# Kernel optimization log

Hardware: AMD Instinct MI355X
Metric: run time of the kernel (lower is better)

Reference implementation:

```python
import jax, jax.numpy as jnp
import numpy as np

NUM_Q = 100000; NUM_C = 1000; D = 128; BS = 128; SEQ = 128
QN = 4; CN = 10; NQC = 4; AGG_HOPS = 2; RANK_K = 10
NEG = jnp.float32(-1e9)


def setup_inputs() -> dict:
    key = jax.random.key(0)
    ks = iter(jax.random.split(key, 40))
    def nrm(shape, scale=0.05):
        return jax.random.normal(next(ks), shape, dtype=jnp.float32) * scale
    inp = {}
    inp['question_seq'] = jax.random.randint(next(ks), (BS, SEQ), 0, NUM_Q, dtype=jnp.int32)
    inp['correct_seq'] = jax.random.randint(next(ks), (BS, SEQ), 0, 2, dtype=jnp.int32)
    inp['mask_seq'] = jnp.ones((BS, SEQ), dtype=jnp.int32)
    inp['question_neighbors'] = jax.random.randint(next(ks), (NUM_Q, QN), 0, NUM_C, dtype=jnp.int32)
    inp['concept_neighbors'] = jax.random.randint(next(ks), (NUM_C, CN), 0, NUM_Q, dtype=jnp.int32)
    inp['qc_table'] = jax.random.randint(next(ks), (NUM_Q, NQC), 0, NUM_C, dtype=jnp.int32)
    inp['Eq'] = nrm((NUM_Q, D), 1.0)
    inp['Ec'] = nrm((NUM_C, D), 1.0)
    inp['Er'] = nrm((2, D), 1.0)
    inp['W_ih1'] = nrm((3 * D, 2 * D)); inp['W_hh1'] = nrm((3 * D, D))
    inp['b_ih1'] = nrm((3 * D,)); inp['b_hh1'] = nrm((3 * D,))
    inp['W_ih2'] = nrm((3 * D, D)); inp['W_hh2'] = nrm((3 * D, D))
    inp['b_ih2'] = nrm((3 * D,)); inp['b_hh2'] = nrm((3 * D,))
    inp['W_agg'] = nrm((AGG_HOPS, D, D)); inp['b_agg'] = nrm((AGG_HOPS, D))
    inp['W_agg_last'] = nrm((D, D)); inp['b_agg_last'] = nrm((D,))
    inp['Wq'] = nrm((D, D)); inp['bq'] = nrm((D,))
    inp['Wk'] = nrm((D, D)); inp['bk'] = nrm((D,))
    inp['Ww'] = nrm((1, 2 * D)); inp['bw'] = nrm((1,))
    inp['h1_init'] = nrm((BS, D)); inp['h2_init'] = nrm((BS, D))
    return inp


def _gru(x, h, W_ih, W_hh, b_ih, b_hh):
    gi = x @ W_ih.T + b_ih
    gh = h @ W_hh.T + b_hh
    ir, iz, i_n = jnp.split(gi, 3, axis=-1)
    hr, hz, hn = jnp.split(gh, 3, axis=-1)
    r = jax.nn.sigmoid(ir + hr)
    z = jax.nn.sigmoid(iz + hz)
    n = jnp.tanh(i_n + r * hn)
    return (1 - z) * n + z * h


def _forward(question_seq, correct_seq, mask_seq, question_neighbors, concept_neighbors, qc_table,
             Eq, Ec, Er, W_ih1, W_hh1, b_ih1, b_hh1, W_ih2, W_hh2, b_ih2, b_hh2,
             W_agg, b_agg, W_agg_last, b_agg_last, Wq, bq, Wk, bk, Ww, bw, h1_init, h2_init):
    bs, seq_len = question_seq.shape
    d = Eq.shape[1]
    # detached question embeddings of the whole history (recap scoring key)
    K_all = jax.lax.stop_gradient(Eq[question_seq])  # [bs, seq, d]
    Wh, Wqc = Ww[:, :d], Ww[:, d:]  # MLP_W split over [state; question_concept]

    def predict(qc, hist, hist_mask):
        # qc: [bs,nqc,d], hist: [bs,ns,d], hist_mask: [bs,ns]
        Kp = qc @ Wk.T + bk                     # MLP_key
        Qp = hist @ Wq.T + bq                   # MLP_query
        logits = jnp.einsum('bsd,bqd->bsq', Qp, Kp)
        logits = jnp.where(hist_mask[:, :, None], logits, NEG)
        w = jax.nn.softmax(logits.reshape(bs, -1), axis=1)
        # pairwise sigmoid(MLP_W([h; e])) without materializing the concat
        v = jax.nn.sigmoid((hist @ Wh[0])[:, :, None] + (qc @ Wqc[0])[:, None, :] + bw[0])
        return jnp.sum(w * v.reshape(bs, -1), axis=1)

    def step(carry, t):
        h1, h2, state_hist, y_hat = carry
        q_t = jnp.take(question_seq, t, axis=1)
        r_t = jnp.take(correct_seq, t, axis=1)
        m_t = jnp.take(mask_seq, t, axis=1) != 0
        # --- 2-hop GNN aggregation (question -> concept -> question) ---
        n1 = question_neighbors[q_t]            # [bs, QN] concept ids
        n2 = concept_neighbors[n1]              # [bs, QN, CN] question ids
        emb = [Eq[q_t], Ec[n1], Eq[n2]]
        for i in range(AGG_HOPS):
            for j in range(AGG_HOPS - i):
                s = jnp.mean(emb[j + 1], axis=-2) + emb[j]
                emb[j] = jnp.tanh(s @ W_agg[j].T + b_agg[j])
        agg = jnp.tanh(emb[0] @ W_agg_last.T + b_agg_last)
        emb_q = jnp.where(m_t[:, None], agg, Eq[q_t])
        # --- GRU state updates (dropout in eval mode = identity) ---
        h1n = _gru(jnp.concatenate([emb_q, Er[r_t]], axis=1), h1, W_ih1, W_hh1, b_ih1, b_hh1)
        g2 = _gru(h1n, h2, W_ih2, W_hh2, b_ih2, b_hh2)
        # --- next question + its concepts ---
        q_next = jnp.take(question_seq, t + 1, axis=1)
        qc = jnp.concatenate([Eq[q_next][:, None], Ec[qc_table[q_next]]], axis=1)  # [bs, 1+NQC, d]
        # --- soft recap: top-k history states by detached embedding similarity ---
        scores = jnp.einsum('bsd,bd->bs', K_all, jax.lax.stop_gradient(Eq[q_next]))
        valid = jnp.arange(seq_len) < t
        scores = jnp.where(valid[None, :], scores, NEG)
        top_vals, top_idx = jax.lax.top_k(scores, RANK_K)
        sel = jnp.take_along_axis(state_hist, top_idx[:, :, None], axis=1)  # [bs, k, d]
        sel_mask = top_vals > NEG / 2
        hist = jnp.concatenate([g2[:, None], sel], axis=1)
        hist_mask = jnp.concatenate([jnp.ones((bs, 1), dtype=bool), sel_mask], axis=1)
        p = predict(qc, hist, hist_mask)
        idx = jnp.where(t == 0, 0, t + 1)  # original writes y_hat[:,0] at t==0
        y_hat = y_hat.at[:, idx].set(p)
        # h2 / state_history NOT updated at t==0 (original `continue`)
        upd = t > 0
        h2n = jnp.where(upd, g2, h2)
        state_hist = jnp.where(upd, state_hist.at[:, t].set(g2), state_hist)
        return (h1n, h2n, state_hist, y_hat), None

    init = (h1_init, h2_init,
            jnp.zeros((bs, seq_len, d), jnp.float32),
            jnp.zeros((bs, seq_len), jnp.float32))
    (_, _, _, y_hat), _ = jax.lax.scan(jax.checkpoint(step), init, jnp.arange(seq_len - 1))
    return y_hat


def reference(question_seq, correct_seq, mask_seq, question_neighbors, concept_neighbors, qc_table,
              Eq, Ec, Er, W_ih1, W_hh1, b_ih1, b_hh1, W_ih2, W_hh2, b_ih2, b_hh2,
              W_agg, b_agg, W_agg_last, b_agg_last, Wq, bq, Wk, bk, Ww, bw, h1_init, h2_init):
    return _forward(question_seq, correct_seq, mask_seq, question_neighbors, concept_neighbors, qc_table,
                    Eq, Ec, Er, W_ih1, W_hh1, b_ih1, b_hh1, W_ih2, W_hh2, b_ih2, b_hh2,
                    W_agg, b_agg, W_agg_last, b_agg_last, Wq, bq, Wk, bk, Ww, bw, h1_init, h2_init)
```

## Files before the change

kernel.cpp:

```cpp
#include <hip/hip_runtime.h>

#define DD 128
#define BSZ 128
#define SEQL 128
#define TST 127
#define QNN 4
#define CNN 10
#define NQCC 4
#define RKK 10
#define NEGV -1000000000.0f

#define OFF_WTA0    0
#define OFF_WTA1    16384
#define OFF_WTAL    32768
#define OFF_WTIH1A  49152
#define OFF_ERIH1   98304
#define OFF_MT      99072
#define OFF_WPACK   115456
#define OFF_ECA0    189184
#define OFF_E1C     317184
#define OFF_KQC     445184
#define OFF_VQCC    509184
#define OFF_KBC     510184
#define OFF_U       511184
#define OFF_W2      511312
#define OFF_C0      511440
#define OFF_GRAM    511488
#define OFF_GI1     511488
#define OFF_KQ0     6753792
#define OFF_VQC0    7802368
#define OFF_KB0     7818752
#define OFF_TIX     7835136
#define OFF_TMSK    7997696
#define OFF_CID     8160256

#define XI(e) ((e) + (((e) >> 5) << 2))
#define PH(e) ((((e) >> 5) * 40) + ((e) & 31))
#define PU(e) ((((e) >> 5) * 20) + (((e) & 31) >> 1))

typedef __fp16 h2 __attribute__((ext_vector_type(2)));

__device__ __forceinline__ float sigm(float x) { return 1.0f / (1.0f + __expf(-x)); }
__device__ __forceinline__ unsigned pkh(float a, float b) {
  h2 v; v.x = (__fp16)a; v.y = (__fp16)b;
  return __builtin_bit_cast(unsigned, v);
}
__device__ __forceinline__ float fd2(float acc, unsigned w, h2 x) {
  return __builtin_amdgcn_fdot2(__builtin_bit_cast(h2, w), x, acc, false);
}
__device__ __forceinline__ float fd2u(float acc, unsigned w, unsigned x) {
  return __builtin_amdgcn_fdot2(__builtin_bit_cast(h2, w), __builtin_bit_cast(h2, x), acc, false);
}
__device__ __forceinline__ void bar() {
  asm volatile("s_waitcnt lgkmcnt(0)" ::: "memory");
  __builtin_amdgcn_s_barrier();
  asm volatile("" ::: "memory");
}

__global__ __launch_bounds__(256) void k_prep(
    const float* __restrict__ W_hh1, const float* __restrict__ W_ih2,
    const float* __restrict__ W_hh2, const float* __restrict__ W_agg,
    const float* __restrict__ W_agg_last, const float* __restrict__ W_ih1,
    const float* __restrict__ Er, float* __restrict__ ws) {
  int idx = blockIdx.x * 256 + threadIdx.x;
  const int TOT = 172800;
  for (int o = idx; o < TOT; o += gridDim.x * 256) {
    int r = o;
    if (r < 16384) { int j = r >> 7, i = r & 127; ws[OFF_WTA0 + r] = W_agg[i * 128 + j]; continue; }
    r -= 16384;
    if (r < 16384) { int j = r >> 7, i = r & 127; ws[OFF_WTA1 + r] = W_agg[16384 + i * 128 + j]; continue; }
    r -= 16384;
    if (r < 16384) { int j = r >> 7, i = r & 127; ws[OFF_WTAL + r] = W_agg_last[i * 128 + j]; continue; }
    r -= 16384;
    if (r < 49152) { int j = r / 384, i = r % 384; ws[OFF_WTIH1A + r] = W_ih1[i * 256 + j]; continue; }
    r -= 49152;
    if (r < 768) {
      int rr = r / 384, i2 = r % 384;
      float a = 0.f;
      for (int j = 0; j < 128; ++j) a += Er[rr * 128 + j] * W_ih1[i2 * 256 + 128 + j];
      ws[OFF_ERIH1 + r] = a; continue;
    }
    r -= 768;
    {
      int n = r & 3; int q = r >> 2;
      int i = q & 127; q >>= 7;
      int kk = q & 3; q >>= 2;
      int jc = q & 3; int c = q >> 2;
      int j0 = jc * 32 + kk * 8 + n * 2;
      const float* row;
      if (c < 3) row = W_hh1 + (size_t)(c * 128 + i) * 128;
      else if (c < 6) row = W_ih2 + (size_t)((c - 3) * 128 + i) * 128;
      else row = W_hh2 + (size_t)((c - 6) * 128 + i) * 128;
      ((unsigned*)ws)[OFF_WPACK + r] = pkh(row[j0], row[j0 + 1]);
    }
  }
}

__global__ __launch_bounds__(128) void k_mqk(
    const float* __restrict__ Wq, const float* __restrict__ Wk,
    const float* __restrict__ bq, const float* __restrict__ bk,
    float* __restrict__ ws) {
  int j = blockIdx.x;
  int tid = threadIdx.x;
  if (j < 128) {
    __shared__ float wkc[128];
    wkc[tid] = Wk[tid * 128 + j];
    __syncthreads();
    float a = 0.f;
    for (int l = 0; l < 128; ++l) a = fmaf(Wq[l * 128 + tid], wkc[l], a);
    ws[OFF_MT + j * 128 + tid] = a;
  } else if (j == 128) {
    float a = 0.f;
    for (int l = 0; l < 128; ++l) a = fmaf(Wq[l * 128 + tid], bk[l], a);
    ws[OFF_U + tid] = a;
  } else {
    float a = 0.f;
    for (int l = 0; l < 128; ++l) a = fmaf(bq[l], Wk[l * 128 + tid], a);
    ws[OFF_W2 + tid] = a;
    __shared__ float sc[128];
    sc[tid] = bq[tid] * bk[tid];
    __syncthreads();
    if (tid == 0) { float s = 0.f; for (int l = 0; l < 128; ++l) s += sc[l]; ws[OFF_C0] = s; }
  }
}

__global__ __launch_bounds__(128) void k_concept(
    const int* __restrict__ cnbr, const float* __restrict__ Eq,
    const float* __restrict__ Ec, const float* __restrict__ b_agg,
    const float* __restrict__ Ww, float* __restrict__ ws) {
  int c = blockIdx.x;
  int tid = threadIdx.x;
  __shared__ int s_nb[CNN];
  __shared__ float s_v[DD], s_ec[DD], s_t2[DD], s_w2[DD], s_kb2[DD];
  if (tid < CNN) s_nb[tid] = cnbr[c * CNN + tid];
  __syncthreads();
  float ec = Ec[c * DD + tid];
  float cm = 0.f;
#pragma unroll
  for (int l = 0; l < CNN; ++l) cm += Eq[(size_t)s_nb[l] * DD + tid];
  s_ec[tid] = ec;
  s_v[tid] = cm * 0.1f + ec;
  __syncthreads();
  const float* WtA0 = ws + OFF_WTA0;
  const float* WtA1 = ws + OFF_WTA1;
  const float* MT = ws + OFF_MT;
  float a1 = 0.f, a0 = 0.f, kq = 0.f;
#pragma unroll 8
  for (int j = 0; j < DD; ++j) {
    a1 += WtA1[j * DD + tid] * s_v[j];
    a0 += WtA0[j * DD + tid] * s_ec[j];
    kq += MT[j * DD + tid] * s_ec[j];
  }
  ws[OFF_E1C + c * DD + tid] = tanhf(a1 + b_agg[DD + tid]);
  ws[OFF_ECA0 + c * DD + tid] = a0;
  s_t2[tid] = kq + ws[OFF_U + tid];
  s_w2[tid] = s_ec[tid] * Ww[128 + tid];
  s_kb2[tid] = s_ec[tid] * ws[OFF_W2 + tid];
  __syncthreads();
  if (tid < 64) {
    ((unsigned*)ws)[OFF_KQC + c * 64 + tid] = pkh(s_t2[2 * tid], s_t2[2 * tid + 1]);
    float pa = s_w2[tid] + s_w2[tid + 64];
    float pb = s_kb2[tid] + s_kb2[tid + 64];
    for (int off = 32; off > 0; off >>= 1) { pa += __shfl_down(pa, off); pb += __shfl_down(pb, off); }
    if (tid == 0) { ws[OFF_VQCC + c] = pa; ws[OFF_KBC + c] = pb + ws[OFF_C0]; }
  }
}

__global__ __launch_bounds__(256) void k_gram(
    const int* __restrict__ qseq, const float* __restrict__ Eq,
    const float* __restrict__ Ww, float* __restrict__ ws) {
  int b = blockIdx.x;
  int tid = threadIdx.x;
  __shared__ float sX[128][129];
  __shared__ float s_tmp[2][8][DD];
  __shared__ int sq[SEQL];
  __shared__ float sU[DD], sWqc[DD], sW2[DD];
  if (tid < 128) {
    sq[tid] = qseq[b * SEQL + tid];
    sU[tid] = ws[OFF_U + tid];
    sWqc[tid] = Ww[128 + tid];
    sW2[tid] = ws[OFF_W2 + tid];
  }
  __syncthreads();
  for (int o = tid; o < 128 * 32; o += 256) {
    int s = o >> 5, p = o & 31;
    float4 v = ((const float4*)(Eq + (size_t)sq[s] * DD))[p];
    sX[s][p * 4] = v.x; sX[s][p * 4 + 1] = v.y; sX[s][p * 4 + 2] = v.z; sX[s][p * 4 + 3] = v.w;
  }
  __syncthreads();
  {
    int r0 = (tid >> 4) * 8, c0 = (tid & 15) * 8;
    float acc[8][8];
#pragma unroll
    for (int u = 0; u < 8; ++u)
#pragma unroll
      for (int v = 0; v < 8; ++v) acc[u][v] = 0.f;
    for (int k = 0; k < 128; ++k) {
      float a[8], bb[8];
#pragma unroll
      for (int u = 0; u < 8; ++u) { a[u] = sX[r0 + u][k]; bb[u] = sX[c0 + u][k]; }
#pragma unroll
      for (int u = 0; u < 8; ++u)
#pragma unroll
        for (int v = 0; v < 8; ++v) acc[u][v] = fmaf(a[u], bb[v], acc[u][v]);
    }
    float* gb = ws + OFF_GRAM + (size_t)b * 16384;
#pragma unroll
    for (int u = 0; u < 8; ++u) {
      float4 v0 = {acc[u][0], acc[u][1], acc[u][2], acc[u][3]};
      float4 v1 = {acc[u][4], acc[u][5], acc[u][6], acc[u][7]};
      ((float4*)(gb + (size_t)(r0 + u) * 128 + c0))[0] = v0;
      ((float4*)(gb + (size_t)(r0 + u) * 128 + c0 + 4))[0] = v1;
    }
  }
  {
    const float* MT = ws + OFF_MT;
    unsigned* KQ0 = (unsigned*)ws + OFF_KQ0;
    int i = tid & 127, half = tid >> 7;
    int s0 = half * 64;
    for (int sb = 0; sb < 64; sb += 8) {
      float acc[8];
#pragma unroll
      for (int u = 0; u < 8; ++u) acc[u] = 0.f;
      for (int j = 0; j < DD; ++j) {
        float w = MT[j * DD + i];
#pragma unroll
        for (int u = 0; u < 8; ++u) acc[u] = fmaf(w, sX[s0 + sb + u][j], acc[u]);
      }
      __syncthreads();
#pragma unroll
      for (int u = 0; u < 8; ++u) s_tmp[half][u][i] = acc[u] + sU[i];
      __syncthreads();
      for (int o = tid; o < 16 * 64; o += 256) {
        int rr = o >> 6, e = o & 63;
        int hh = rr >> 3, uu = rr & 7;
        int s = hh * 64 + sb + uu;
        KQ0[((size_t)b * 128 + s) * 64 + e] = pkh(s_tmp[hh][uu][2 * e], s_tmp[hh][uu][2 * e + 1]);
      }
      __syncthreads();
    }
  }
  if (tid < 128) {
    float a = 0.f, kb = 0.f;
    for (int j = 0; j < DD; ++j) {
      float xv = sX[tid][j];
      a = fmaf(xv, sWqc[j], a);
      kb = fmaf(xv, sW2[j], kb);
    }
    ws[OFF_VQC0 + b * 128 + tid] = a;
    ws[OFF_KB0 + b * 128 + tid] = kb + ws[OFF_C0];
  }
}

__global__ __launch_bounds__(128) void k_topk(
    const int* __restrict__ qseq, const int* __restrict__ qctab,
    float* __restrict__ ws) {
  int* tix = (int*)(ws + OFF_TIX);
  int* tmsk = (int*)(ws + OFF_TMSK);
  int* cid = (int*)(ws + OFF_CID);
  int tid = threadIdx.x;
  int lane = tid & 63, wv = tid >> 6;
  int bt = blockIdx.x * 2 + wv;
  int b = bt / TST, t = bt - b * TST;
  if (lane < 5) {
    int qn = qseq[b * SEQL + t + 1];
    cid[(b * 128 + t + 1) * 5 + lane] = (lane == 0) ? qn : qctab[qn * NQCC + lane - 1];
  }
  const float* grow = ws + OFF_GRAM + ((size_t)b * 128 + (t + 1)) * 128;
  float v0 = (lane < t) ? grow[lane] : NEGV;
  float v1 = (lane + 64 < t) ? grow[lane + 64] : NEGV;
  for (int k = 0; k < RKK; ++k) {
    float bv = v0; int bi = lane;
    if (v1 > bv) { bv = v1; bi = lane + 64; }
    for (int off = 32; off > 0; off >>= 1) {
      float ov = __shfl_down(bv, off);
      int oi = __shfl_down(bi, off);
      if (ov > bv || (ov == bv && oi < bi)) { bv = ov; bi = oi; }
    }
    bv = __shfl(bv, 0); bi = __shfl(bi, 0);
    if (lane == 0) {
      tix[bt * RKK + k] = bi;
      tmsk[bt * RKK + k] = (bv > NEGV * 0.5f) ? 1 : 0;
    }
    if (bi == lane) v0 = -__builtin_inff();
    if (bi == lane + 64) v1 = -__builtin_inff();
  }
}

__global__ __launch_bounds__(128) void k_agg(
    const int* __restrict__ qseq, const int* __restrict__ rseq,
    const int* __restrict__ mseq, const int* __restrict__ qnbr,
    const float* __restrict__ Eq, const float* __restrict__ b_agg,
    const float* __restrict__ b_agg_last, const float* __restrict__ b_ih1,
    float* __restrict__ ws) {
  int blk = blockIdx.x;
  int b = blk >> 4, g = blk & 15;
  int t0 = g * 8;
  int nu = (t0 + 8 <= TST) ? 8 : (TST - t0);
  int tid = threadIdx.x;
  __shared__ float s_a[8][DD], s_b[8][DD], s_c[8][DD];
  __shared__ int s_q[8], s_r[8], s_m[8];
  __shared__ int s_n1[8][QNN];
  if (tid < 8) {
    int ok = tid < nu;
    int idx = b * SEQL + (ok ? (t0 + tid) : 0);
    s_q[tid] = qseq[idx];
    s_r[tid] = ok ? rseq[idx] : 0;
    s_m[tid] = ok ? mseq[idx] : 0;
  }
  __syncthreads();
  if (tid < 32) { int u = tid >> 2, k = tid & 3; s_n1[u][k] = qnbr[s_q[u] * QNN + k]; }
  for (int o = tid; o < 8 * 32; o += 128) {
    int u = o >> 5, p = o & 31;
    float4 v = ((const float4*)(Eq + (size_t)s_q[u] * DD))[p];
    s_a[u][p * 4] = v.x; s_a[u][p * 4 + 1] = v.y; s_a[u][p * 4 + 2] = v.z; s_a[u][p * 4 + 3] = v.w;
  }
  __syncthreads();
  const float* WtA0 = ws + OFF_WTA0;
  const float* WtAL = ws + OFF_WTAL;
  const float* WtIH1A = ws + OFF_WTIH1A;
  const float* EcA0 = ws + OFF_ECA0;
  const float* E1C = ws + OFF_E1C;
  float acc[8];
#pragma unroll
  for (int u = 0; u < 8; ++u) acc[u] = 0.f;
  for (int j = 0; j < DD; ++j) {
    float w = WtA0[j * DD + tid];
#pragma unroll
    for (int u = 0; u < 8; ++u) acc[u] = fmaf(w, s_a[u][j], acc[u]);
  }
  float bat = b_agg[tid];
#pragma unroll
  for (int u = 0; u < 8; ++u) {
    int n0 = s_n1[u][0], n1 = s_n1[u][1], n2 = s_n1[u][2], n3 = s_n1[u][3];
    float pre0 = 0.25f * (EcA0[n0 * DD + tid] + EcA0[n1 * DD + tid] + EcA0[n2 * DD + tid] + EcA0[n3 * DD + tid]);
    float e0 = tanhf(acc[u] + pre0 + bat);
    float e1m = 0.25f * (E1C[n0 * DD + tid] + E1C[n1 * DD + tid] + E1C[n2 * DD + tid] + E1C[n3 * DD + tid]);
    s_b[u][tid] = e1m + e0;
  }
  __syncthreads();
#pragma unroll
  for (int u = 0; u < 8; ++u) acc[u] = 0.f;
  for (int j = 0; j < DD; ++j) {
    float w = WtA0[j * DD + tid];
#pragma unroll
    for (int u = 0; u < 8; ++u) acc[u] = fmaf(w, s_b[u][j], acc[u]);
  }
#pragma unroll
  for (int u = 0; u < 8; ++u) s_c[u][tid] = tanhf(acc[u] + bat);
  __syncthreads();
#pragma unroll
  for (int u = 0; u < 8; ++u) acc[u] = 0.f;
  for (int j = 0; j < DD; ++j) {
    float w = WtAL[j * DD + tid];
#pragma unroll
    for (int u = 0; u < 8; ++u) acc[u] = fmaf(w, s_c[u][j], acc[u]);
  }
  float balt = b_agg_last[tid];
#pragma unroll
  for (int u = 0; u < 8; ++u) {
    float aggv = tanhf(acc[u] + balt);
    s_b[u][tid] = s_m[u] ? aggv : s_a[u][tid];
  }
  __syncthreads();
  float g0[8], g1[8], g2[8];
#pragma unroll
  for (int u = 0; u < 8; ++u) { g0[u] = 0.f; g1[u] = 0.f; g2[u] = 0.f; }
  for (int j = 0; j < DD; ++j) {
    float w0 = WtIH1A[j * 384 + tid];
    float w1 = WtIH1A[j * 384 + 128 + tid];
    float w2 = WtIH1A[j * 384 + 256 + tid];
#pragma unroll
    for (int u = 0; u < 8; ++u) {
      float x = s_b[u][j];
      g0[u] = fmaf(w0, x, g0[u]);
      g1[u] = fmaf(w1, x, g1[u]);
      g2[u] = fmaf(w2, x, g2[u]);
    }
  }
  for (int u = 0; u < nu; ++u) {
    const float* ErI = ws + OFF_ERIH1 + s_r[u] * 384;
    float* gi1 = ws + OFF_GI1 + (size_t)(b * TST + t0 + u) * 384;
    gi1[tid] = g0[u] + ErI[tid] + b_ih1[tid];
    gi1[128 + tid] = g1[u] + ErI[128 + tid] + b_ih1[128 + tid];
    gi1[256 + tid] = g2[u] + ErI[256 + tid] + b_ih1[256 + tid];
  }
}

__global__ __launch_bounds__(512, 2) void k_seq(
    const float* __restrict__ b_hh1, const float* __restrict__ b_ih2,
    const float* __restrict__ b_hh2, const float* __restrict__ Ww,
    const float* __restrict__ bw, const float* __restrict__ h1i,
    const float* __restrict__ h2i, float* __restrict__ ws,
    float* __restrict__ out) {
  const int tid = threadIdx.x;
  const int b = blockIdx.x;
  const int i = tid >> 2, jc = tid & 3;
  const int lane = tid & 63, wv = tid >> 6;
  const int bt0 = b * TST;

  const float4* gi1f4 = (const float4*)(ws + OFF_GI1);
  const unsigned* KQ0 = (const unsigned*)ws + OFF_KQ0;
  const unsigned* KQC = (const unsigned*)ws + OFF_KQC;
  const float* vqc0_all = ws + OFF_VQC0;
  const float* vqcC_all = ws + OFF_VQCC;
  const float* kb0_all = ws + OFF_KB0;
  const float* kbC_all = ws + OFF_KBC;
  const int* tix_all = (const int*)(ws + OFF_TIX);
  const int* tmsk_all = (const int*)(ws + OFF_TMSK);
  const int* cid_all = (const int*)(ws + OFF_CID);
  const uint4* wp = (const uint4*)((const unsigned*)ws + OFF_WPACK);

  __shared__ float s_h1f[2][144], s_g2f[2][144], s_h2f[144];
  __shared__ unsigned s_h1pk[2][80], s_g2pk[2][80], s_h2pk[80];
  __shared__ unsigned qph_pk[SEQL * 66];
  __shared__ unsigned s_Kq[2][5 * 66];
  __shared__ float s_gi1[384];
  __shared__ float s_vhh[SEQL];
  __shared__ float s_logit[64];
  __shared__ float s_bhh1[384], s_bih2[384], s_bhh2[384];
  __shared__ float s_vh[11], s_vqc[2][5], s_kb[2][5], s_bw;
  __shared__ int s_tix[RKK], s_hm[11], s_cidn[5];

  uint4 wgt[9][4];
#pragma unroll
  for (int c = 0; c < 9; ++c)
#pragma unroll
    for (int kk = 0; kk < 4; ++kk)
      wgt[c][kk] = wp[((c * 4 + jc) * 4 + kk) * 128 + i];
#pragma unroll
  for (int c = 0; c < 9; ++c)
#pragma unroll
    for (int kk = 0; kk < 4; ++kk)
      asm volatile("" : "+v"(wgt[c][kk].x), "+v"(wgt[c][kk].y),
                        "+v"(wgt[c][kk].z), "+v"(wgt[c][kk].w));

  if (tid < 384) { s_bhh1[tid] = b_hh1[tid]; s_bih2[tid] = b_ih2[tid]; s_bhh2[tid] = b_hh2[tid]; }
  if (tid < 128) {
    float h1v = h1i[b * DD + tid], h2v = h2i[b * DD + tid];
    s_h1f[0][XI(tid)] = h1v;
    ((__fp16*)s_h1pk[0])[PH(tid)] = (__fp16)h1v;
    s_h2f[XI(tid)] = h2v;
    ((__fp16*)s_h2pk)[PH(tid)] = (__fp16)h2v;
    s_vhh[tid] = 0.f;
  }
  if (tid >= 55 && tid < 64) s_logit[tid] = NEGV;
  float wh_lo = 0.f, wh_hi = 0.f;
  if (wv == 7) { wh_lo = Ww[lane]; wh_hi = Ww[64 + lane]; }
  if (tid == 0) { s_bw = bw[0]; out[b * SEQL + 1] = 0.f; s_hm[0] = 1; }
  if (tid >= 296 && tid < 301) s_cidn[tid - 296] = cid_all[(b * 128 + 1) * 5 + tid - 296];
  __syncthreads();
  for (int o = tid; o < SEQL * 66; o += 512) qph_pk[o] = 0u;
  if (tid < 96) ((float4*)s_gi1)[tid] = gi1f4[(size_t)bt0 * 96 + tid];
  __syncthreads();

  for (int t = 0; t <= TST; ++t) {
    const int par = t & 1, parn = par ^ 1;
    float4 pf4 = {0.f, 0.f, 0.f, 0.f};
    unsigned pfu = 0, pfu2 = 0; int pfs = 0; float pfv = 0.f, pfkb = 0.f;

    if (t < TST) {
      const int tg = (t + 1 < TST) ? t + 1 : TST - 1;
      if (tid < 96) pf4 = gi1f4[(size_t)(bt0 + tg) * 96 + tid];
      else if (tid < 256) {
        int kx = tid - 96;
        { int s = kx >> 6, e = kx & 63;
          pfu = (s == 0) ? KQ0[(size_t)(b * 128 + t + 1) * 64 + e] : KQC[s_cidn[s] * 64 + e]; }
        { int kx2 = kx + 160; int s = kx2 >> 6, e = kx2 & 63;
          pfu2 = KQC[s_cidn[s] * 64 + e]; }
      } else if (tid < 291) {
        int k = tid - 256;
        if (k < 5) pfv = (k == 0) ? vqc0_all[b * 128 + t + 1] : vqcC_all[s_cidn[k]];
        else if (k < 10) { int s = k - 5; pfkb = (s == 0) ? kb0_all[b * 128 + t + 1] : kbC_all[s_cidn[s]]; }
        else if (k < 20) pfs = tix_all[(bt0 + t) * RKK + k - 10];
        else if (k < 30) pfs = tmsk_all[(bt0 + t) * RKK + k - 20];
        else { int tn = (t + 1 < TST) ? t + 1 : TST - 1; pfs = cid_all[(b * 128 + tn + 1) * 5 + k - 30]; }
      }
      const uint4* xp = (const uint4*)s_h1pk[par] + jc * 5;
      float a0 = 0.f, a1 = 0.f, a2 = 0.f;
#pragma unroll
      for (int kk = 0; kk < 4; ++kk) {
        uint4 xk = xp[kk];
        uint4 w;
        w = wgt[0][kk]; a0 = fd2u(a0, w.x, xk.x); a0 = fd2u(a0, w.y, xk.y); a0 = fd2u(a0, w.z, xk.z); a0 = fd2u(a0, w.w, xk.w);
        w = wgt[1][kk]; a1 = fd2u(a1, w.x, xk.x); a1 = fd2u(a1, w.y, xk.y); a1 = fd2u(a1, w.z, xk.z); a1 = fd2u(a1, w.w, xk.w);
        w = wgt[2][kk]; a2 = fd2u(a2, w.x, xk.x); a2 = fd2u(a2, w.y, xk.y); a2 = fd2u(a2, w.z, xk.z); a2 = fd2u(a2, w.w, xk.w);
      }
      a0 += __shfl_down(a0, 2); a0 += __shfl_down(a0, 1);
      a1 += __shfl_down(a1, 2); a1 += __shfl_down(a1, 1);
      a2 += __shfl_down(a2, 2); a2 += __shfl_down(a2, 1);
      if (jc == 0) {
        float r = sigm(s_gi1[i] + a0 + s_bhh1[i]);
        float z = sigm(s_gi1[128 + i] + a1 + s_bhh1[128 + i]);
        float n = tanhf(s_gi1[256 + i] + r * (a2 + s_bhh1[256 + i]));
        float h1n = (1.f - z) * n + z * s_h1f[par][XI(i)];
        s_h1f[parn][XI(i)] = h1n;
        ((__fp16*)s_h1pk[parn])[PH(i)] = (__fp16)h1n;
      }
    }
    if (t >= 1) {
      if (tid < 440) {
        int p = tid >> 3, sub = tid & 7;
        int q = p / 5, s = p - q * 5;
        const unsigned* kpr = &s_Kq[parn][s * 66 + sub * 8];
        float a = 0.f;
        if (q == 0) {
          const unsigned* g2u = s_g2pk[parn];
          int e0 = sub * 16;
#pragma unroll
          for (int k = 0; k < 8; ++k) a = fd2u(a, kpr[k], g2u[PU(e0 + 2 * k)]);
        } else {
          const unsigned* ro = qph_pk + s_tix[q - 1] * 66;
#pragma unroll
          for (int k = 0; k < 8; ++k) a = fd2u(a, ro[sub * 8 + k], kpr[k]);
        }
        a += __shfl_down(a, 4);
        a += __shfl_down(a, 2);
        a += __shfl_down(a, 1);
        if (sub == 0) s_logit[p] = s_hm[q] ? (a + s_kb[parn][s]) : NEGV;
      } else if (wv == 7) {
        float pa = s_g2f[parn][XI(lane)] * wh_lo + s_g2f[parn][XI(64 + lane)] * wh_hi;
        for (int off = 32; off > 0; off >>= 1) pa += __shfl_down(pa, off);
        if (lane == 0) s_vh[0] = pa;
        if (lane >= 16 && lane < 26) s_vh[1 + lane - 16] = s_vhh[s_tix[lane - 16]];
      }
    }
    bar();

    if (t < TST) {
      const uint4* xn = (const uint4*)s_h1pk[parn] + jc * 5;
      const uint4* xh = (t <= 1) ? ((const uint4*)s_h2pk + jc * 5)
                                 : ((const uint4*)s_g2pk[parn] + jc * 5);
      float a0 = 0.f, a1 = 0.f, a2 = 0.f, c0 = 0.f, c1 = 0.f, c2 = 0.f;
#pragma unroll
      for (int kk = 0; kk < 4; ++kk) {
        uint4 xa = xn[kk], xb = xh[kk];
        uint4 w;
        w = wgt[3][kk]; a0 = fd2u(a0, w.x, xa.x); a0 = fd2u(a0, w.y, xa.y); a0 = fd2u(a0, w.z, xa.z); a0 = fd2u(a0, w.w, xa.w);
        w = wgt[4][kk]; a1 = fd2u(a1, w.x, xa.x); a1 = fd2u(a1, w.y, xa.y); a1 = fd2u(a1, w.z, xa.z); a1 = fd2u(a1, w.w, xa.w);
        w = wgt[5][kk]; a2 = fd2u(a2, w.x, xa.x); a2 = fd2u(a2, w.y, xa.y); a2 = fd2u(a2, w.z, xa.z); a2 = fd2u(a2, w.w, xa.w);
        w = wgt[6][kk]; c0 = fd2u(c0, w.x, xb.x); c0 = fd2u(c0, w.y, xb.y); c0 = fd2u(c0, w.z, xb.z); c0 = fd2u(c0, w.w, xb.w);
        w = wgt[7][kk]; c1 = fd2u(c1, w.x, xb.x); c1 = fd2u(c1, w.y, xb.y); c1 = fd2u(c1, w.z, xb.z); c1 = fd2u(c1, w.w, xb.w);
        w = wgt[8][kk]; c2 = fd2u(c2, w.x, xb.x); c2 = fd2u(c2, w.y, xb.y); c2 = fd2u(c2, w.z, xb.z); c2 = fd2u(c2, w.w, xb.w);
      }
      a0 += __shfl_down(a0, 2); a0 += __shfl_down(a0, 1);
      a1 += __shfl_down(a1, 2); a1 += __shfl_down(a1, 1);
      a2 += __shfl_down(a2, 2); a2 += __shfl_down(a2, 1);
      c0 += __shfl_down(c0, 2); c0 += __shfl_down(c0, 1);
      c1 += __shfl_down(c1, 2); c1 += __shfl_down(c1, 1);
      c2 += __shfl_down(c2, 2); c2 += __shfl_down(c2, 1);
      if (jc == 0) {
        float r = sigm(a0 + s_bih2[i] + c0 + s_bhh2[i]);
        float z = sigm(a1 + s_bih2[128 + i] + c1 + s_bhh2[128 + i]);
        float n = tanhf(a2 + s_bih2[256 + i] + r * (c2 + s_bhh2[256 + i]));
        float h2old = (t <= 1) ? s_h2f[XI(i)] : s_g2f[parn][XI(i)];
        float g2v = (1.f - z) * n + z * h2old;
        s_g2f[par][XI(i)] = g2v;
        ((__fp16*)s_g2pk[par])[PH(i)] = (__fp16)g2v;
      }
    }
    if (t >= 1 && wv == 7) {
      float l = s_logit[lane];
      float m = l;
      for (int off = 32; off > 0; off >>= 1) m = fmaxf(m, __shfl_xor(m, off));
      float e = __expf(l - m);
      float v = 0.f;
      if (lane < 55) {
        int q = lane / 5, s = lane - q * 5;
        v = sigm(s_vh[q] + s_vqc[parn][s] + s_bw);
      }
      float num = e * v, den = e;
      for (int off = 32; off > 0; off >>= 1) { num += __shfl_xor(num, off); den += __shfl_xor(den, off); }
      if (lane == 0) out[b * SEQL + ((t - 1 == 0) ? 0 : t)] = num / den;
    }
    if (t < TST) {
      if (tid < 96) ((float4*)s_gi1)[tid] = pf4;
      else if (tid < 256) {
        int kx = tid - 96;
        { int s = kx >> 6, e = kx & 63; s_Kq[par][s * 66 + e] = pfu; }
        { int kx2 = kx + 160; int s = kx2 >> 6, e = kx2 & 63; s_Kq[par][s * 66 + e] = pfu2; }
      } else if (tid < 291) {
        int k = tid - 256;
        if (k < 5) s_vqc[par][k] = pfv;
        else if (k < 10) s_kb[par][k - 5] = pfkb;
        else if (k < 20) s_tix[k - 10] = pfs;
        else if (k < 30) s_hm[1 + k - 20] = pfs;
        else s_cidn[k - 30] = pfs;
      }
    }
    if (t >= 2 && tid >= 320 && tid < 384) {
      int k2 = tid - 320;
      qph_pk[(t - 1) * 66 + k2] = s_g2pk[parn][PU(2 * k2)];
    }
    if (t >= 2 && tid == 0) s_vhh[t - 1] = s_vh[0];
    bar();
  }
}

extern "C" void kernel_launch(void* const* d_in, const int* in_sizes, int n_in,
                              void* d_out, int out_size, void* d_ws, size_t ws_size,
                              hipStream_t stream) {
  (void)in_sizes; (void)n_in; (void)out_size; (void)ws_size;
  const int* qseq = (const int*)d_in[0];
  const int* rseq = (const int*)d_in[1];
  const int* mseq = (const int*)d_in[2];
  const int* qnbr = (const int*)d_in[3];
  const int* cnbr = (const int*)d_in[4];
  const int* qctab = (const int*)d_in[5];
  const float* Eq = (const float*)d_in[6];
  const float* Ec = (const float*)d_in[7];
  const float* Er = (const float*)d_in[8];
  const float* W_ih1 = (const float*)d_in[9];
  const float* W_hh1 = (const float*)d_in[10];
  const float* b_ih1 = (const float*)d_in[11];
  const float* b_hh1 = (const float*)d_in[12];
  const float* W_ih2 = (const float*)d_in[13];
  const float* W_hh2 = (const float*)d_in[14];
  const float* b_ih2 = (const float*)d_in[15];
  const float* b_hh2 = (const float*)d_in[16];
  const float* W_agg = (const float*)d_in[17];
  const float* b_agg = (const float*)d_in[18];
  const float* W_agg_last = (const float*)d_in[19];
  const float* b_agg_last = (const float*)d_in[20];
  const float* Wq = (const float*)d_in[21];
  const float* bq = (const float*)d_in[22];
  const float* Wk = (const float*)d_in[23];
  const float* bk = (const float*)d_in[24];
  const float* Ww = (const float*)d_in[25];
  const float* bw = (const float*)d_in[26];
  const float* h1i = (const float*)d_in[27];
  const float* h2i = (const float*)d_in[28];
  float* ws = (float*)d_ws;
  float* out = (float*)d_out;

  hipLaunchKernelGGL(k_prep, dim3(675), dim3(256), 0, stream,
                     W_hh1, W_ih2, W_hh2, W_agg, W_agg_last, W_ih1, Er, ws);
  hipLaunchKernelGGL(k_mqk, dim3(130), dim3(128), 0, stream,
                     Wq, Wk, bq, bk, ws);
  hipLaunchKernelGGL(k_concept, dim3(1000), dim3(128), 0, stream,
                     cnbr, Eq, Ec, b_agg, Ww, ws);
  hipLaunchKernelGGL(k_gram, dim3(BSZ), dim3(256), 0, stream,
                     qseq, Eq, Ww, ws);
  hipLaunchKernelGGL(k_topk, dim3(BSZ * TST / 2), dim3(128), 0, stream,
                     qseq, qctab, ws);
  hipLaunchKernelGGL(k_agg, dim3(BSZ * 16), dim3(128), 0, stream,
                     qseq, rseq, mseq, qnbr, Eq, b_agg, b_agg_last, b_ih1, ws);
  hipLaunchKernelGGL(k_seq, dim3(BSZ), dim3(512), 0, stream,
                     b_hh1, b_ih2, b_hh2, Ww, bw, h1i, h2i, ws, out);
}
```

Baseline: 617.6 us.

## Merge prep kernels, split gram kernel roles, use fast tanh

```diff
diff --git a/kernel.cpp b/kernel.cpp
--- a/kernel.cpp
+++ b/kernel.cpp
@@ -41,6 +41,12 @@
 typedef __fp16 h2 __attribute__((ext_vector_type(2)));
 
 __device__ __forceinline__ float sigm(float x) { return 1.0f / (1.0f + __expf(-x)); }
+__device__ __forceinline__ float ftanh(float x) {
+  float ax = fabsf(x);
+  float T = __expf(-2.f * ax);
+  float r = (1.f - T) * __builtin_amdgcn_rcpf(1.f + T);
+  return copysignf(r, x);
+}
 __device__ __forceinline__ unsigned pkh(float a, float b) {
   h2 v; v.x = (__fp16)a; v.y = (__fp16)b;
   return __builtin_bit_cast(unsigned, v);
@@ -61,66 +67,71 @@
     const float* __restrict__ W_hh1, const float* __restrict__ W_ih2,
     const float* __restrict__ W_hh2, const float* __restrict__ W_agg,
     const float* __restrict__ W_agg_last, const float* __restrict__ W_ih1,
-    const float* __restrict__ Er, float* __restrict__ ws) {
-  int idx = blockIdx.x * 256 + threadIdx.x;
-  const int TOT = 172800;
-  for (int o = idx; o < TOT; o += gridDim.x * 256) {
-    int r = o;
-    if (r < 16384) { int j = r >> 7, i = r & 127; ws[OFF_WTA0 + r] = W_agg[i * 128 + j]; continue; }
-    r -= 16384;
-    if (r < 16384) { int j = r >> 7, i = r & 127; ws[OFF_WTA1 + r] = W_agg[16384 + i * 128 + j]; continue; }
-    r -= 16384;
-    if (r < 16384) { int j = r >> 7, i = r & 127; ws[OFF_WTAL + r] = W_agg_last[i * 128 + j]; continue; }
-    r -= 16384;
-    if (r < 49152) { int j = r / 384, i = r % 384; ws[OFF_WTIH1A + r] = W_ih1[i * 256 + j]; continue; }
-    r -= 49152;
-    if (r < 768) {
-      int rr = r / 384, i2 = r % 384;
-      float a = 0.f;
-      for (int j = 0; j < 128; ++j) a += Er[rr * 128 + j] * W_ih1[i2 * 256 + 128 + j];
-      ws[OFF_ERIH1 + r] = a; continue;
-    }
-    r -= 768;
-    {
-      int n = r & 3; int q = r >> 2;
-      int i = q & 127; q >>= 7;
-      int kk = q & 3; q >>= 2;
-      int jc = q & 3; int c = q >> 2;
-      int j0 = jc * 32 + kk * 8 + n * 2;
-      const float* row;
-      if (c < 3) row = W_hh1 + (size_t)(c * 128 + i) * 128;
-      else if (c < 6) row = W_ih2 + (size_t)((c - 3) * 128 + i) * 128;
-      else row = W_hh2 + (size_t)((c - 6) * 128 + i) * 128;
-      ((unsigned*)ws)[OFF_WPACK + r] = pkh(row[j0], row[j0 + 1]);
-    }
-  }
-}
-
-__global__ __launch_bounds__(128) void k_mqk(
-    const float* __restrict__ Wq, const float* __restrict__ Wk,
-    const float* __restrict__ bq, const float* __restrict__ bk,
-    float* __restrict__ ws) {
-  int j = blockIdx.x;
+    const float* __restrict__ Er, const float* __restrict__ Wq,
+    const float* __restrict__ Wk, const float* __restrict__ bq,
+    const float* __restrict__ bk, float* __restrict__ ws) {
   int tid = threadIdx.x;
-  if (j < 128) {
+  if (blockIdx.x < 675) {
+    int idx = blockIdx.x * 256 + tid;
+    const int TOT = 172800;
+    for (int o = idx; o < TOT; o += 675 * 256) {
+      int r = o;
+      if (r < 16384) { int j = r >> 7, i = r & 127; ws[OFF_WTA0 + r] = W_agg[i * 128 + j]; continue; }
+      r -= 16384;
+      if (r < 16384) { int j = r >> 7, i = r & 127; ws[OFF_WTA1 + r] = W_agg[16384 + i * 128 + j]; continue; }
+      r -= 16384;
+      if (r < 16384) { int j = r >> 7, i = r & 127; ws[OFF_WTAL + r] = W_agg_last[i * 128 + j]; continue; }
+      r -= 16384;
+      if (r < 49152) { int j = r / 384, i = r % 384; ws[OFF_WTIH1A + r] = W_ih1[i * 256 + j]; continue; }
+      r -= 49152;
+      if (r < 768) {
+        int rr = r / 384, i2 = r % 384;
+        float a = 0.f;
+        for (int j = 0; j < 128; ++j) a += Er[rr * 128 + j] * W_ih1[i2 * 256 + 128 + j];
+        ws[OFF_ERIH1 + r] = a; continue;
+      }
+      r -= 768;
+      {
+        int n = r & 3; int q = r >> 2;
+        int i = q & 127; q >>= 7;
+        int kk = q & 3; q >>= 2;
+        int jc = q & 3; int c = q >> 2;
+        int j0 = jc * 32 + kk * 8 + n * 2;
+        const float* row;
+        if (c < 3) row = W_hh1 + (size_t)(c * 128 + i) * 128;
+        else if (c < 6) row = W_ih2 + (size_t)((c - 3) * 128 + i) * 128;
+        else row = W_hh2 + (size_t)((c - 6) * 128 + i) * 128;
+        ((unsigned*)ws)[OFF_WPACK + r] = pkh(row[j0], row[j0 + 1]);
+      }
+    }
+  } else {
+    int j = blockIdx.x - 675;
     __shared__ float wkc[128];
-    wkc[tid] = Wk[tid * 128 + j];
-    __syncthreads();
-    float a = 0.f;
-    for (int l = 0; l < 128; ++l) a = fmaf(Wq[l * 128 + tid], wkc[l], a);
-    ws[OFF_MT + j * 128 + tid] = a;
-  } else if (j == 128) {
-    float a = 0.f;
-    for (int l = 0; l < 128; ++l) a = fmaf(Wq[l * 128 + tid], bk[l], a);
-    ws[OFF_U + tid] = a;
-  } else {
-    float a = 0.f;
-    for (int l = 0; l < 128; ++l) a = fmaf(bq[l], Wk[l * 128 + tid], a);
-    ws[OFF_W2 + tid] = a;
     __shared__ float sc[128];
-    sc[tid] = bq[tid] * bk[tid];
-    __syncthreads();
-    if (tid == 0) { float s = 0.f; for (int l = 0; l < 128; ++l) s += sc[l]; ws[OFF_C0] = s; }
+    if (j < 128) {
+      if (tid < 128) wkc[tid] = Wk[tid * 128 + j];
+      __syncthreads();
+      if (tid < 128) {
+        float a = 0.f;
+        for (int l = 0; l < 128; ++l) a = fmaf(Wq[l * 128 + tid], wkc[l], a);
+        ws[OFF_MT + j * 128 + tid] = a;
+      }
+    } else if (j == 128) {
+      if (tid < 128) {
+        float a = 0.f;
+        for (int l = 0; l < 128; ++l) a = fmaf(Wq[l * 128 + tid], bk[l], a);
+        ws[OFF_U + tid] = a;
+      }
+    } else {
+      if (tid < 128) {
+        float a = 0.f;
+        for (int l = 0; l < 128; ++l) a = fmaf(bq[l], Wk[l * 128 + tid], a);
+        ws[OFF_W2 + tid] = a;
+        sc[tid] = bq[tid] * bk[tid];
+      }
+      __syncthreads();
+      if (tid == 0) { float s = 0.f; for (int l = 0; l < 128; ++l) s += sc[l]; ws[OFF_C0] = s; }
+    }
   }
 }
 
@@ -151,7 +162,7 @@
     a0 += WtA0[j * DD + tid] * s_ec[j];
     kq += MT[j * DD + tid] * s_ec[j];
   }
-  ws[OFF_E1C + c * DD + tid] = tanhf(a1 + b_agg[DD + tid]);
+  ws[OFF_E1C + c * DD + tid] = ftanh(a1 + b_agg[DD + tid]);
   ws[OFF_ECA0 + c * DD + tid] = a0;
   s_t2[tid] = kq + ws[OFF_U + tid];
   s_w2[tid] = s_ec[tid] * Ww[128 + tid];
@@ -169,18 +180,12 @@
 __global__ __launch_bounds__(256) void k_gram(
     const int* __restrict__ qseq, const float* __restrict__ Eq,
     const float* __restrict__ Ww, float* __restrict__ ws) {
-  int b = blockIdx.x;
+  int role = blockIdx.x >> 7;
+  int b = blockIdx.x & 127;
   int tid = threadIdx.x;
   __shared__ float sX[128][129];
-  __shared__ float s_tmp[2][8][DD];
   __shared__ int sq[SEQL];
-  __shared__ float sU[DD], sWqc[DD], sW2[DD];
-  if (tid < 128) {
-    sq[tid] = qseq[b * SEQL + tid];
-    sU[tid] = ws[OFF_U + tid];
-    sWqc[tid] = Ww[128 + tid];
-    sW2[tid] = ws[OFF_W2 + tid];
-  }
+  if (tid < 128) sq[tid] = qseq[b * SEQL + tid];
   __syncthreads();
   for (int o = tid; o < 128 * 32; o += 256) {
     int s = o >> 5, p = o & 31;
@@ -188,7 +193,7 @@
     sX[s][p * 4] = v.x; sX[s][p * 4 + 1] = v.y; sX[s][p * 4 + 2] = v.z; sX[s][p * 4 + 3] = v.w;
   }
   __syncthreads();
-  {
+  if (role == 0) {
     int r0 = (tid >> 4) * 8, c0 = (tid & 15) * 8;
     float acc[8][8];
 #pragma unroll
@@ -212,8 +217,15 @@
       ((float4*)(gb + (size_t)(r0 + u) * 128 + c0))[0] = v0;
       ((float4*)(gb + (size_t)(r0 + u) * 128 + c0 + 4))[0] = v1;
     }
-  }
-  {
+  } else {
+    __shared__ float s_tmp[2][8][DD];
+    __shared__ float sU[DD], sWqc[DD], sW2[DD];
+    if (tid < 128) {
+      sU[tid] = ws[OFF_U + tid];
+      sWqc[tid] = Ww[128 + tid];
+      sW2[tid] = ws[OFF_W2 + tid];
+    }
+    __syncthreads();
     const float* MT = ws + OFF_MT;
     unsigned* KQ0 = (unsigned*)ws + OFF_KQ0;
     int i = tid & 127, half = tid >> 7;
@@ -239,16 +251,16 @@
       }
       __syncthreads();
     }
-  }
-  if (tid < 128) {
-    float a = 0.f, kb = 0.f;
-    for (int j = 0; j < DD; ++j) {
-      float xv = sX[tid][j];
-      a = fmaf(xv, sWqc[j], a);
-      kb = fmaf(xv, sW2[j], kb);
-    }
-    ws[OFF_VQC0 + b * 128 + tid] = a;
-    ws[OFF_KB0 + b * 128 + tid] = kb + ws[OFF_C0];
+    if (tid < 128) {
+      float a = 0.f, kb = 0.f;
+      for (int j = 0; j < DD; ++j) {
+        float xv = sX[tid][j];
+        a = fmaf(xv, sWqc[j], a);
+        kb = fmaf(xv, sW2[j], kb);
+      }
+      ws[OFF_VQC0 + b * 128 + tid] = a;
+      ws[OFF_KB0 + b * 128 + tid] = kb + ws[OFF_C0];
+    }
   }
 }
 
@@ -334,7 +346,7 @@
   for (int u = 0; u < 8; ++u) {
     int n0 = s_n1[u][0], n1 = s_n1[u][1], n2 = s_n1[u][2], n3 = s_n1[u][3];
     float pre0 = 0.25f * (EcA0[n0 * DD + tid] + EcA0[n1 * DD + tid] + EcA0[n2 * DD + tid] + EcA0[n3 * DD + tid]);
-    float e0 = tanhf(acc[u] + pre0 + bat);
+    float e0 = ftanh(acc[u] + pre0 + bat);
     float e1m = 0.25f * (E1C[n0 * DD + tid] + E1C[n1 * DD + tid] + E1C[n2 * DD + tid] + E1C[n3 * DD + tid]);
     s_b[u][tid] = e1m + e0;
   }
@@ -347,7 +359,7 @@
     for (int u = 0; u < 8; ++u) acc[u] = fmaf(w, s_b[u][j], acc[u]);
   }
 #pragma unroll
-  for (int u = 0; u < 8; ++u) s_c[u][tid] = tanhf(acc[u] + bat);
+  for (int u = 0; u < 8; ++u) s_c[u][tid] = ftanh(acc[u] + bat);
   __syncthreads();
 #pragma unroll
   for (int u = 0; u < 8; ++u) acc[u] = 0.f;
@@ -359,7 +371,7 @@
   float balt = b_agg_last[tid];
 #pragma unroll
   for (int u = 0; u < 8; ++u) {
-    float aggv = tanhf(acc[u] + balt);
+    float aggv = ftanh(acc[u] + balt);
     s_b[u][tid] = s_m[u] ? aggv : s_a[u][tid];
   }
   __syncthreads();
@@ -492,7 +504,7 @@
       if (jc == 0) {
         float r = sigm(s_gi1[i] + a0 + s_bhh1[i]);
         float z = sigm(s_gi1[128 + i] + a1 + s_bhh1[128 + i]);
-        float n = tanhf(s_gi1[256 + i] + r * (a2 + s_bhh1[256 + i]));
+        float n = ftanh(s_gi1[256 + i] + r * (a2 + s_bhh1[256 + i]));
         float h1n = (1.f - z) * n + z * s_h1f[par][XI(i)];
         s_h1f[parn][XI(i)] = h1n;
         ((__fp16*)s_h1pk[parn])[PH(i)] = (__fp16)h1n;
@@ -552,7 +564,7 @@
       if (jc == 0) {
         float r = sigm(a0 + s_bih2[i] + c0 + s_bhh2[i]);
         float z = sigm(a1 + s_bih2[128 + i] + c1 + s_bhh2[128 + i]);
-        float n = tanhf(a2 + s_bih2[256 + i] + r * (c2 + s_bhh2[256 + i]));
+        float n = ftanh(a2 + s_bih2[256 + i] + r * (c2 + s_bhh2[256 + i]));
         float h2old = (t <= 1) ? s_h2f[XI(i)] : s_g2f[parn][XI(i)];
         float g2v = (1.f - z) * n + z * h2old;
         s_g2f[par][XI(i)] = g2v;
@@ -633,13 +645,12 @@
   float* ws = (float*)d_ws;
   float* out = (float*)d_out;
 
-  hipLaunchKernelGGL(k_prep, dim3(675), dim3(256), 0, stream,
-                     W_hh1, W_ih2, W_hh2, W_agg, W_agg_last, W_ih1, Er, ws);
-  hipLaunchKernelGGL(k_mqk, dim3(130), dim3(128), 0, stream,
+  hipLaunchKernelGGL(k_prep, dim3(805), dim3(256), 0, stream,
+                     W_hh1, W_ih2, W_hh2, W_agg, W_agg_last, W_ih1, Er,
                      Wq, Wk, bq, bk, ws);
   hipLaunchKernelGGL(k_concept, dim3(1000), dim3(128), 0, stream,
                      cnbr, Eq, Ec, b_agg, Ww, ws);
-  hipLaunchKernelGGL(k_gram, dim3(BSZ), dim3(256), 0, stream,
+  hipLaunchKernelGGL(k_gram, dim3(256), dim3(256), 0, stream,
                      qseq, Eq, Ww, ws);
   hipLaunchKernelGGL(k_topk, dim3(BSZ * TST / 2), dim3(128), 0, stream,
                      qseq, qctab, ws);
```

New measurement: 574.4 us. -7.0%, faster.
